# Performance work log

Measured on AMD Instinct MI355X. Metric: run time of the kernel, lower is better.

## Reference

```python
import jax, jax.numpy as jnp
import numpy as np

N_NODES = 50000
N_EDGES = 1600000
D = 64  # per-node feature dim for h1 and h2


def setup_inputs() -> dict:
    key = jax.random.key(0)
    ks = jax.random.split(key, 8)
    h1 = jax.random.normal(ks[0], (N_NODES, D), dtype=jnp.float32)
    h2 = jax.random.normal(ks[1], (N_NODES, D), dtype=jnp.float32)
    src = jax.random.randint(ks[2], (N_EDGES,), 0, N_NODES)
    dst = jax.random.randint(ks[3], (N_EDGES,), 0, N_NODES)
    # MLP params: layer_sizes = [256, 128, 128, 1]
    def glorot(k, fan_in, fan_out):
        lim = (6.0 / (fan_in + fan_out)) ** 0.5
        return jax.random.uniform(k, (fan_in, fan_out), jnp.float32, -lim, lim)
    W0 = glorot(ks[4], 4 * D, 128)
    W1 = glorot(ks[5], 128, 128)
    W2 = glorot(ks[6], 128, 1)
    b0 = jnp.zeros((128,), jnp.float32)
    b1 = jnp.zeros((128,), jnp.float32)
    b2 = jnp.zeros((1,), jnp.float32)
    return {"h1": h1, "h2": h2, "src": src, "dst": dst,
            "W0": W0, "b0": b0, "W1": W1, "b1": b1, "W2": W2, "b2": b2}


def reference(h1, h2, src, dst, W0, b0, W1, b1, W2, b2):
    # Edge-wise gather of src/dst node features, concat -> MLP (eval mode: dropout=identity).
    h = jnp.concatenate([h1[src], h1[dst], h2[src], h2[dst]], axis=1)  # [E, 4D]
    h = h @ W0 + b0
    h = jax.nn.relu(h) @ W1 + b1
    h = jax.nn.relu(h) @ W2 + b2
    return h  # [E, out_features]
```

## Files before the change

kernel.cpp:

```cpp
#include <hip/hip_runtime.h>
#include <hip/hip_bf16.h>
#include <stdint.h>


typedef __attribute__((ext_vector_type(8))) __bf16 bf16x8;
typedef __attribute__((ext_vector_type(8))) _Float16 f16x8;
typedef __attribute__((ext_vector_type(4))) _Float16 f16x4;
typedef __attribute__((ext_vector_type(4))) float  floatx4;

__device__ inline floatx4 mfma_bf16(bf16x8 a, bf16x8 b, floatx4 c) {
  return __builtin_amdgcn_mfma_f32_16x16x32_bf16(a, b, c, 0, 0, 0);
}
__device__ inline floatx4 mfma_f16(f16x8 a, f16x8 b, floatx4 c) {
  return __builtin_amdgcn_mfma_f32_16x16x32_f16(a, b, c, 0, 0, 0);
}

__device__ inline void bar_lds() {
  asm volatile("s_waitcnt lgkmcnt(0)" ::: "memory");
  __builtin_amdgcn_s_barrier();
}

__global__ void cvt_w_kernel(const float* __restrict__ W0, const float* __restrict__ W1,
                             _Float16* __restrict__ W1T, __bf16* __restrict__ W0uT,
                             __bf16* __restrict__ W0wT) {
  const int t = blockIdx.x * 256 + threadIdx.x;
  if (t < 16384) {
    const int n = t >> 7, k = t & 127;
    W1T[t] = (_Float16)W1[k * 128 + n];
  } else if (t < 32768) {
    const int t2 = t - 16384;
    const int n = t2 >> 7, k2 = t2 & 127;
    const int row = (k2 < 64) ? k2 : 64 + k2;
    W0uT[t2] = (__bf16)W0[row * 128 + n];
  } else {
    const int t3 = t - 32768;
    const int n = t3 >> 7, k2 = t3 & 127;
    const int row = (k2 < 64) ? 64 + k2 : 128 + k2;
    W0wT[t3] = (__bf16)W0[row * 128 + n];
  }
}

__global__ __launch_bounds__(256, 2)
void node_uw_kernel(const float* __restrict__ h1, const float* __restrict__ h2,
                    const __bf16* __restrict__ W0uT, const __bf16* __restrict__ W0wT,
                    const float* __restrict__ b0,
                    _Float16* __restrict__ uTab, _Float16* __restrict__ wTab,
                    int nNodes) {
  __shared__ char sN[64 * 256];
  const int tid = threadIdx.x;
  const int base = blockIdx.x * 64;

  {
    const int r = tid >> 2, q = tid & 3;
    const int node = base + r;
    const int swz = (r & 7) << 4;
#pragma unroll
    for (int ii = 0; ii < 4; ++ii) {
      const int c = q * 4 + ii;
      bf16x8 v;
      if (node < nNodes) {
        const float* sp = (c < 8) ? (h1 + (size_t)node * 64 + c * 8)
                                  : (h2 + (size_t)node * 64 + (c - 8) * 8);
        const float4 x = reinterpret_cast<const float4*>(sp)[0];
        const float4 y = reinterpret_cast<const float4*>(sp)[1];
        v[0] = (__bf16)x.x; v[1] = (__bf16)x.y; v[2] = (__bf16)x.z; v[3] = (__bf16)x.w;
        v[4] = (__bf16)y.x; v[5] = (__bf16)y.y; v[6] = (__bf16)y.z; v[7] = (__bf16)y.w;
      } else {
#pragma unroll
        for (int k = 0; k < 8; ++k) v[k] = (__bf16)0.f;
      }
      *reinterpret_cast<bf16x8*>(sN + r * 256 + ((c * 16) ^ swz)) = v;
    }
  }
  __syncthreads();

  const int lane = tid & 63;
  const int l15 = lane & 15;
  const int hi = lane >> 4;
  const int hi16 = hi * 16;
  const int wvU = __builtin_amdgcn_readfirstlane(tid >> 6);

  float b0c[2][4];
#pragma unroll
  for (int nt = 0; nt < 2; ++nt)
#pragma unroll
    for (int r = 0; r < 4; ++r) b0c[nt][r] = b0[wvU * 32 + nt * 16 + hi * 4 + r];

#pragma unroll
  for (int pass = 0; pass < 2; ++pass) {
    const __bf16* Wt = pass ? W0wT : W0uT;
    _Float16* Tab = pass ? wTab : uTab;
    const bf16x8* wp = reinterpret_cast<const bf16x8*>(Wt);
    bf16x8 wf[4][2];
#pragma unroll
    for (int kk = 0; kk < 4; ++kk) {
      wf[kk][0] = wp[(wvU * 32 + l15) * 16 + kk * 4 + hi];
      wf[kk][1] = wp[(wvU * 32 + 16 + l15) * 16 + kk * 4 + hi];
    }
    floatx4 acc[4][2];
#pragma unroll
    for (int mt = 0; mt < 4; ++mt) { acc[mt][0] = (floatx4)0.f; acc[mt][1] = (floatx4)0.f; }
#pragma unroll
    for (int kk = 0; kk < 4; ++kk) {
#pragma unroll
      for (int mt = 0; mt < 4; ++mt) {
        const int row = mt * 16 + l15;
        const bf16x8 a = *reinterpret_cast<const bf16x8*>(
            sN + row * 256 + ((kk * 64 + hi16) ^ ((row & 7) << 4)));
        acc[mt][0] = mfma_bf16(wf[kk][0], a, acc[mt][0]);
        acc[mt][1] = mfma_bf16(wf[kk][1], a, acc[mt][1]);
      }
    }
#pragma unroll
    for (int mt = 0; mt < 4; ++mt) {
      const int node = base + mt * 16 + l15;
      if (node < nNodes) {
#pragma unroll
        for (int nt = 0; nt < 2; ++nt) {
          f16x4 pk;
#pragma unroll
          for (int r = 0; r < 4; ++r) {
            const float v = acc[mt][nt][r] + (pass ? 0.f : b0c[nt][r]);
            pk[r] = (_Float16)v;
          }
          *reinterpret_cast<f16x4*>(Tab + (size_t)node * 128 + wvU * 32 + nt * 16 +
                                    hi * 4) = pk;
        }
      }
    }
  }
}

__global__ __launch_bounds__(512, 2)
void edge_uw_kernel(const _Float16* __restrict__ uTab, const _Float16* __restrict__ wTab,
                    const int* __restrict__ srcI, const int* __restrict__ dstI,
                    const _Float16* __restrict__ W1T, const float* __restrict__ b1,
                    const float* __restrict__ W2, const float* __restrict__ b2,
                    float* __restrict__ out, int E, int nTiles) {
  __shared__ char sUW[2 * 64 * 512];
  __shared__ char sH[64 * 256];

  const int tid = threadIdx.x;
  const int lane = tid & 63;
  const int l15 = lane & 15;
  const int hi = lane >> 4;
  const int hi16 = hi * 16;
  const int wvU = __builtin_amdgcn_readfirstlane(tid >> 6);
  const int wm = wvU >> 2;
  const int wn = wvU & 3;

  const int lhalf = lane >> 5;
  const int p31 = lane & 31;
  const int half = (p31 >> 4) & 1;
  const int* gIdxTab = half ? dstI : srcI;
  const _Float16* gTab = half ? wTab : uTab;

  f16x8 w1f[4][2];
  const f16x8* w1p = reinterpret_cast<const f16x8*>(W1T);
#pragma unroll
  for (int kk = 0; kk < 4; ++kk) {
    w1f[kk][0] = w1p[(wn * 32 + l15) * 16 + kk * 4 + hi];
    w1f[kk][1] = w1p[(wn * 32 + 16 + l15) * 16 + kk * 4 + hi];
  }
  float b1c[2][4], w2c[2][4];
#pragma unroll
  for (int nt = 0; nt < 2; ++nt)
#pragma unroll
    for (int r = 0; r < 4; ++r) {
      const int n = wn * 32 + nt * 16 + hi * 4 + r;
      b1c[nt][r] = b1[n];
      w2c[nt][r] = W2[n];
    }
  const float b2v = b2[0];

  const int tstride = gridDim.x;

  auto loadIdx = [&](int (&d)[4], int tt2) {
    const bool valid = tt2 < nTiles;
#pragma unroll
    for (int i = 0; i < 4; ++i) {
      const int eLoc = wvU * 8 + i * 2 + lhalf;
      const int ge = tt2 * 64 + eLoc;
      d[i] = (valid && ge < E) ? gIdxTab[ge] : 0;
    }
  };

  auto issueGather = [&](int nb, const int (&idx4)[4]) {
#pragma unroll
    for (int i = 0; i < 4; ++i) {
      const int eLoc = wvU * 8 + i * 2 + lhalf;
      const int wc = (p31 & 8) | ((p31 & 7) ^ (eLoc & 7));
      const _Float16* g = gTab + (size_t)idx4[i] * 128 + wc * 8;
      char* l = sUW + nb * 32768 + wvU * 4096 + i * 1024;
      __builtin_amdgcn_global_load_lds(
          (const __attribute__((address_space(1))) void*)g,
          (__attribute__((address_space(3))) void*)l, 16, 0, 0);
    }
  };

  const int tile0 = blockIdx.x;
  int idxA[4], idxB[4];
  loadIdx(idxA, tile0);
  issueGather(0, idxA);
  loadIdx(idxB, tile0 + tstride);
  int cur = 0;

  for (int tt = tile0; tt < nTiles; tt += tstride) {
    __syncthreads();

    if (tt + tstride < nTiles) issueGather(cur ^ 1, idxB);
    loadIdx(idxA, tt + 2 * tstride);

    char* sUWc = sUW + cur * 32768;

    {
      const int aR = tid >> 3;
      const int q = tid & 7;
      const int aswz = (aR & 7) << 4;
      const char* rowU = sUWc + aR * 512;
      char* rowH = sH + aR * 256;
#pragma unroll
      for (int ii = 0; ii < 2; ++ii) {
        const int c = q * 2 + ii;
        const int off = (c * 16) ^ aswz;
        const f16x8 uu = *reinterpret_cast<const f16x8*>(rowU + off);
        const f16x8 ww = *reinterpret_cast<const f16x8*>(rowU + 256 + off);
        f16x8 hh = uu + ww;
#pragma unroll
        for (int k = 0; k < 8; ++k)
          hh[k] = hh[k] > (_Float16)0 ? hh[k] : (_Float16)0;
        *reinterpret_cast<f16x8*>(rowH + off) = hh;
      }
    }
    bar_lds();

    floatx4 acc2T[2][2];
#pragma unroll
    for (int mt = 0; mt < 2; ++mt) { acc2T[mt][0] = (floatx4)0.f; acc2T[mt][1] = (floatx4)0.f; }
#pragma unroll
    for (int kk = 0; kk < 4; ++kk) {
#pragma unroll
      for (int mt = 0; mt < 2; ++mt) {
        const int row = wm * 32 + mt * 16 + l15;
        const f16x8 a = *reinterpret_cast<const f16x8*>(
            sH + row * 256 + ((kk * 64 + hi16) ^ ((row & 7) << 4)));
        acc2T[mt][0] = mfma_f16(w1f[kk][0], a, acc2T[mt][0]);
        acc2T[mt][1] = mfma_f16(w1f[kk][1], a, acc2T[mt][1]);
      }
    }

    float* sRedF = (float*)sUWc;
#pragma unroll
    for (int mt = 0; mt < 2; ++mt) {
      float pp = 0.f;
#pragma unroll
      for (int nt = 0; nt < 2; ++nt)
#pragma unroll
        for (int r = 0; r < 4; ++r)
          pp += fmaxf(acc2T[mt][nt][r] + b1c[nt][r], 0.0f) * w2c[nt][r];
      pp += __shfl_xor(pp, 16);
      pp += __shfl_xor(pp, 32);
      if (lane < 16) sRedF[(wm * 32 + mt * 16 + l15) * 4 + wn] = pp;
    }
    bar_lds();

    if (tid < 64) {
      const int ge = tt * 64 + tid;
      if (ge < E) {
        const float4 v = reinterpret_cast<const float4*>(sRedF)[tid];
        out[ge] = v.x + v.y + v.z + v.w + b2v;
      }
    }

#pragma unroll
    for (int i = 0; i < 4; ++i) idxB[i] = idxA[i];
    cur ^= 1;
  }
}

__global__ void edge_mlp_fallback(const float* __restrict__ h1, const float* __restrict__ h2,
                                  const int* __restrict__ src, const int* __restrict__ dst,
                                  const float* __restrict__ W0, const float* __restrict__ b0,
                                  const float* __restrict__ W1, const float* __restrict__ b1,
                                  const float* __restrict__ W2, const float* __restrict__ b2,
                                  float* __restrict__ out, int E) {
  __shared__ float sa[256];
  __shared__ float sh[128];
  __shared__ float sr[128];
  const int e = blockIdx.x;
  if (e >= E) return;
  const int t = threadIdx.x;
  const int is = src[e], id = dst[e];
  if (t < 64) { sa[t] = h1[is * 64 + t]; sa[128 + t] = h2[is * 64 + t]; }
  else { const int u = t - 64; sa[64 + u] = h1[id * 64 + u]; sa[192 + u] = h2[id * 64 + u]; }
  __syncthreads();
  float a0 = b0[t];
  for (int k = 0; k < 256; ++k) a0 += sa[k] * W0[k * 128 + t];
  sh[t] = fmaxf(a0, 0.f);
  __syncthreads();
  float a1 = b1[t];
  for (int k = 0; k < 128; ++k) a1 += sh[k] * W1[k * 128 + t];
  sr[t] = fmaxf(a1, 0.f) * W2[t];
  __syncthreads();
  if (t == 0) {
    float s = b2[0];
    for (int k = 0; k < 128; ++k) s += sr[k];
    out[e] = s;
  }
}

extern "C" void kernel_launch(void* const* d_in, const int* in_sizes, int n_in,
                              void* d_out, int out_size, void* d_ws, size_t ws_size,
                              hipStream_t stream) {
  const float* h1 = (const float*)d_in[0];
  const float* h2 = (const float*)d_in[1];
  const int* src = (const int*)d_in[2];
  const int* dst = (const int*)d_in[3];
  const float* W0 = (const float*)d_in[4];
  const float* b0 = (const float*)d_in[5];
  const float* W1 = (const float*)d_in[6];
  const float* b1 = (const float*)d_in[7];
  const float* W2 = (const float*)d_in[8];
  const float* b2 = (const float*)d_in[9];
  float* out = (float*)d_out;

  const int D = 64;
  const int nNodes = in_sizes[0] / D;
  const int E = in_sizes[2];

  char* ws = (char*)d_ws;
  _Float16* W1T = (_Float16*)(ws);
  __bf16* W0uT = (__bf16*)(ws + 32768);
  __bf16* W0wT = (__bf16*)(ws + 65536);
  const size_t tabBytes = (size_t)nNodes * 128 * sizeof(_Float16);
  _Float16* uTab = (_Float16*)(ws + 98304);
  _Float16* wTab = (_Float16*)(ws + 98304 + tabBytes);
  const bool useFast = ws_size >= 98304 + 2 * tabBytes;

  if (!useFast) {
    edge_mlp_fallback<<<dim3(E), dim3(128), 0, stream>>>(
        h1, h2, src, dst, W0, b0, W1, b1, W2, b2, out, E);
    return;
  }

  cvt_w_kernel<<<dim3(192), dim3(256), 0, stream>>>(W0, W1, W1T, W0uT, W0wT);
  node_uw_kernel<<<dim3((nNodes + 63) / 64), dim3(256), 0, stream>>>(
      h1, h2, W0uT, W0wT, b0, uTab, wTab, nNodes);

  const int nTiles = (E + 63) / 64;
  const int grid = nTiles < 512 ? nTiles : 512;
  edge_uw_kernel<<<dim3(grid), dim3(512), 0, stream>>>(
      uTab, wTab, src, dst, W1T, b1, W2, b2, out, E, nTiles);
}
```

Measured before the change: 139.9 us.

## Fuse add+ReLU into MFMA operand loads, drop sH buffer, remap waves to 4x2

Each wave now builds its layer-2 A operand directly from the gathered u/w rows in registers (add + ReLU) and feeds it straight to the MFMAs. This removes the intermediate sH LDS buffer, its stores and one barrier per tile. Waves are regrouped from a 2x4 to a 4x2 grid, so each holds 16 W1 fragments and b1/W2 are kept in packed half precision to save registers. Launch bounds are raised to 4 blocks per CU, relying on the smaller LDS footprint. The trade-off is more register pressure per wave, a risk of spills under the tighter occupancy target, and b1/W2 rounded to fp16.

```diff
diff --git a/kernel.cpp b/kernel.cpp
--- a/kernel.cpp
+++ b/kernel.cpp
@@ -131,14 +131,14 @@
   }
 }
 
-__global__ __launch_bounds__(512, 2)
+__global__ __launch_bounds__(512, 4)
 void edge_uw_kernel(const _Float16* __restrict__ uTab, const _Float16* __restrict__ wTab,
                     const int* __restrict__ srcI, const int* __restrict__ dstI,
                     const _Float16* __restrict__ W1T, const float* __restrict__ b1,
                     const float* __restrict__ W2, const float* __restrict__ b2,
                     float* __restrict__ out, int E, int nTiles) {
   __shared__ char sUW[2 * 64 * 512];
-  __shared__ char sH[64 * 256];
+  __shared__ __align__(8) float sRed[64][2];
 
   const int tid = threadIdx.x;
   const int lane = tid & 63;
@@ -146,8 +146,8 @@
   const int hi = lane >> 4;
   const int hi16 = hi * 16;
   const int wvU = __builtin_amdgcn_readfirstlane(tid >> 6);
-  const int wm = wvU >> 2;
-  const int wn = wvU & 3;
+  const int wm = wvU >> 1;
+  const int wn = wvU & 1;
 
   const int lhalf = lane >> 5;
   const int p31 = lane & 31;
@@ -155,21 +155,22 @@
   const int* gIdxTab = half ? dstI : srcI;
   const _Float16* gTab = half ? wTab : uTab;
 
-  f16x8 w1f[4][2];
+  f16x8 w1f[4][4];
   const f16x8* w1p = reinterpret_cast<const f16x8*>(W1T);
 #pragma unroll
-  for (int kk = 0; kk < 4; ++kk) {
-    w1f[kk][0] = w1p[(wn * 32 + l15) * 16 + kk * 4 + hi];
-    w1f[kk][1] = w1p[(wn * 32 + 16 + l15) * 16 + kk * 4 + hi];
-  }
-  float b1c[2][4], w2c[2][4];
-#pragma unroll
-  for (int nt = 0; nt < 2; ++nt)
+  for (int kk = 0; kk < 4; ++kk)
+#pragma unroll
+    for (int nt = 0; nt < 4; ++nt)
+      w1f[kk][nt] = w1p[(wn * 64 + nt * 16 + l15) * 16 + kk * 4 + hi];
+
+  f16x4 b1h[4], w2h[4];
+#pragma unroll
+  for (int nt = 0; nt < 4; ++nt)
 #pragma unroll
     for (int r = 0; r < 4; ++r) {
-      const int n = wn * 32 + nt * 16 + hi * 4 + r;
-      b1c[nt][r] = b1[n];
-      w2c[nt][r] = W2[n];
+      const int n = wn * 64 + nt * 16 + hi * 4 + r;
+      b1h[nt][r] = (_Float16)b1[n];
+      w2h[nt][r] = (_Float16)W2[n];
     }
   const float b2v = b2[0];
 
@@ -211,64 +212,48 @@
     if (tt + tstride < nTiles) issueGather(cur ^ 1, idxB);
     loadIdx(idxA, tt + 2 * tstride);
 
-    char* sUWc = sUW + cur * 32768;
-
+    const char* sUWc = sUW + cur * 32768;
+
+    floatx4 acc2T[4];
+#pragma unroll
+    for (int nt = 0; nt < 4; ++nt) acc2T[nt] = (floatx4)0.f;
     {
-      const int aR = tid >> 3;
-      const int q = tid & 7;
-      const int aswz = (aR & 7) << 4;
-      const char* rowU = sUWc + aR * 512;
-      char* rowH = sH + aR * 256;
-#pragma unroll
-      for (int ii = 0; ii < 2; ++ii) {
-        const int c = q * 2 + ii;
-        const int off = (c * 16) ^ aswz;
+      const int row = wm * 16 + l15;
+      const char* rowU = sUWc + row * 512;
+      const int rswz = (row & 7) << 4;
+#pragma unroll
+      for (int kk = 0; kk < 4; ++kk) {
+        const int off = (kk * 64 + hi16) ^ rswz;
         const f16x8 uu = *reinterpret_cast<const f16x8*>(rowU + off);
         const f16x8 ww = *reinterpret_cast<const f16x8*>(rowU + 256 + off);
         f16x8 hh = uu + ww;
 #pragma unroll
         for (int k = 0; k < 8; ++k)
           hh[k] = hh[k] > (_Float16)0 ? hh[k] : (_Float16)0;
-        *reinterpret_cast<f16x8*>(rowH + off) = hh;
-      }
-    }
-    bar_lds();
-
-    floatx4 acc2T[2][2];
-#pragma unroll
-    for (int mt = 0; mt < 2; ++mt) { acc2T[mt][0] = (floatx4)0.f; acc2T[mt][1] = (floatx4)0.f; }
-#pragma unroll
-    for (int kk = 0; kk < 4; ++kk) {
-#pragma unroll
-      for (int mt = 0; mt < 2; ++mt) {
-        const int row = wm * 32 + mt * 16 + l15;
-        const f16x8 a = *reinterpret_cast<const f16x8*>(
-            sH + row * 256 + ((kk * 64 + hi16) ^ ((row & 7) << 4)));
-        acc2T[mt][0] = mfma_f16(w1f[kk][0], a, acc2T[mt][0]);
-        acc2T[mt][1] = mfma_f16(w1f[kk][1], a, acc2T[mt][1]);
-      }
-    }
-
-    float* sRedF = (float*)sUWc;
-#pragma unroll
-    for (int mt = 0; mt < 2; ++mt) {
+#pragma unroll
+        for (int nt = 0; nt < 4; ++nt)
+          acc2T[nt] = mfma_f16(w1f[kk][nt], hh, acc2T[nt]);
+      }
+    }
+
+    {
       float pp = 0.f;
 #pragma unroll
-      for (int nt = 0; nt < 2; ++nt)
+      for (int nt = 0; nt < 4; ++nt)
 #pragma unroll
         for (int r = 0; r < 4; ++r)
-          pp += fmaxf(acc2T[mt][nt][r] + b1c[nt][r], 0.0f) * w2c[nt][r];
+          pp += fmaxf(acc2T[nt][r] + (float)b1h[nt][r], 0.0f) * (float)w2h[nt][r];
       pp += __shfl_xor(pp, 16);
       pp += __shfl_xor(pp, 32);
-      if (lane < 16) sRedF[(wm * 32 + mt * 16 + l15) * 4 + wn] = pp;
+      if (lane < 16) sRed[wm * 16 + l15][wn] = pp;
     }
     bar_lds();
 
     if (tid < 64) {
       const int ge = tt * 64 + tid;
       if (ge < E) {
-        const float4 v = reinterpret_cast<const float4*>(sRedF)[tid];
-        out[ge] = v.x + v.y + v.z + v.w + b2v;
+        const float2 v = *reinterpret_cast<const float2*>(&sRed[tid][0]);
+        out[ge] = v.x + v.y + b2v;
       }
     }
 
```

Measured after the change: 241.7 us. +72.7%, slower.
